# Kernel tuning notes

Hardware: AMD Instinct MI355X
Metric: run time of the kernel (lower is better)

## Reference

```python
import jax, jax.numpy as jnp
from jax import lax
import numpy as np

B, N_VARS, M_CLAUSES, K_DIM = 1024, 64, 256, 12
MAX_ITER = 12


def setup_inputs() -> dict:
    key = jax.random.key(0)
    k1, k2, k3, k4 = jax.random.split(key, 4)
    z = jax.random.uniform(k1, (B, N_VARS), dtype=jnp.float32)          # input probabilities
    S = jax.random.normal(k2, (M_CLAUSES, N_VARS + 1), dtype=jnp.float32) * 0.2  # learnable clause matrix (col 0 = truth var)
    w = jax.random.uniform(k3, (M_CLAUSES,), dtype=jnp.float32)          # learnable clause weights
    r = jax.random.normal(k4, (B, N_VARS, K_DIM), dtype=jnp.float32)     # random init directions
    return {"z": z, "S": S, "w": w, "r": r, "max_iter": MAX_ITER}


def _mixing(z, S, w, r, max_iter):
    Bsz, n = z.shape
    m, N = S.shape  # N = n + 1 (truth variable is column 0)
    k = r.shape[-1]
    eps = jnp.float32(1e-8)

    # truth direction v_T = e_0
    vT = jnp.zeros((k,), dtype=z.dtype).at[0].set(1.0)

    # random unit directions orthogonal to v_T (zero out component along e_0)
    r_perp = r.at[..., 0].set(0.0)
    r_perp = r_perp / jnp.maximum(jnp.linalg.norm(r_perp, axis=-1, keepdims=True), eps)

    # SATNet init: v_i = -cos(pi z_i) v_T + sin(pi z_i) r_perp_i
    ang = jnp.pi * z
    Vvars = -jnp.cos(ang)[..., None] * vT + jnp.sin(ang)[..., None] * r_perp  # [B,n,k]
    V = jnp.concatenate([jnp.broadcast_to(vT, (Bsz, 1, k)), Vvars], axis=1)   # [B,N,k]

    Sw = S * w[:, None]                       # weighted clause matrix [m,N]
    W = jnp.einsum('mn,bnk->bmk', Sw, V)      # running product Sw @ V, [B,m,k]
    snrm = jnp.sum(Sw * Sw, axis=0)           # ||s_i||^2 per variable, [N]

    def coord_step(carry, i):
        V, W = carry
        s_i = Sw[:, i]                         # [m]
        v_old = V[:, i, :]                     # [B,k]
        g = jnp.einsum('bmk,m->bk', W, s_i) - snrm[i] * v_old
        v_new = -g / jnp.maximum(jnp.linalg.norm(g, axis=-1, keepdims=True), eps)
        W = W + (v_new - v_old)[:, None, :] * s_i[None, :, None]  # rank-1 update
        V = V.at[:, i, :].set(v_new)
        return (V, W), None

    def sweep(carry, _):
        carry, _ = lax.scan(coord_step, carry, jnp.arange(1, N))  # coordinate descent over variables
        return carry, None

    (V, _), _ = lax.scan(sweep, (V, W), None, length=max_iter)

    # output probabilities: z_i = arccos(-v_i . v_T) / pi
    cos = jnp.clip(-V[:, 1:, 0], -1.0 + 1e-6, 1.0 - 1e-6)
    return jnp.arccos(cos) / jnp.pi


def reference(z, S, w, r, max_iter):
    return _mixing(z, S, w, r, max_iter)
```

## Files before the change

kernel.cpp:

```cpp
#include <hip/hip_runtime.h>
#include <math.h>

#define BATCH 1024
#define NV    64
#define MC    256
#define KD    12
#define PI_F  3.14159265358979323846f

#define CBUF  4480
#define C0OFF 4352
#define DGOFF 4416

template <int CTRL>
__device__ __forceinline__ float dpp_addf(float x) {
  int y = __builtin_amdgcn_update_dpp(0, __float_as_int(x), CTRL, 0xF, 0xF, true);
  return x + __int_as_float(y);
}
__device__ __forceinline__ float allreduce16(float x) {
  x = dpp_addf<0xB1>(x);
  x = dpp_addf<0x4E>(x);
  x = dpp_addf<0x124>(x);
  x = dpp_addf<0x128>(x);
  return x;
}
__device__ __forceinline__ float readlane63(float x) {
  return __int_as_float(__builtin_amdgcn_readlane(__float_as_int(x), 63));
}

__global__ void compute_C_kernel(const float* __restrict__ S,
                                 const float* __restrict__ w,
                                 float* __restrict__ Cg, int nsplit) {
  const int q = blockIdx.x;
  const int mc = blockIdx.y;
  const int j = threadIdx.x;
  if (j > NV) return;
  const int v = (q + 1) % 64 + 1;
  const int mlen = MC / nsplit;
  const int m0 = mc * mlen;
  float a0 = 0.f, a1 = 0.f, a2 = 0.f, a3 = 0.f;
  for (int m = m0; m < m0 + mlen; m += 4) {
    const float w0 = w[m], w1 = w[m + 1], w2 = w[m + 2], w3 = w[m + 3];
    a0 = fmaf(S[(m + 0) * (NV + 1) + v] * w0 * w0, S[(m + 0) * (NV + 1) + j], a0);
    a1 = fmaf(S[(m + 1) * (NV + 1) + v] * w1 * w1, S[(m + 1) * (NV + 1) + j], a1);
    a2 = fmaf(S[(m + 2) * (NV + 1) + v] * w2 * w2, S[(m + 2) * (NV + 1) + j], a2);
    a3 = fmaf(S[(m + 3) * (NV + 1) + v] * w3 * w3, S[(m + 3) * (NV + 1) + j], a3);
  }
  const float acc = (a0 + a1) + (a2 + a3);
  float* buf = Cg + mc * CBUF;
  if (j == 0) buf[C0OFF + q] = acc;
  else        buf[q * 68 + (j - 1)] = acc;
  const int pv = (v == 1) ? 64 : (v - 1);
  if (j == pv) buf[DGOFF + (v - 1)] = acc;
}

__global__ __launch_bounds__(256, 1) void mixing_kernel(
    const float* __restrict__ z, const float* __restrict__ r,
    const float* __restrict__ Cg, const int* __restrict__ max_iter_p,
    float* __restrict__ out, int nsplit) {
  __shared__ float Ls[CBUF];

  const int t = threadIdx.x;
  const int l = t & 63;
  const int kq = l >> 4;
  const int n16 = l & 15;
  const int b = blockIdx.x * 4 + (t >> 6);
  const int max_iter = max_iter_p[0];

  {
    const float4* src = (const float4*)Cg;
    float4* dst = (float4*)Ls;
    for (int idx = t; idx < CBUF / 4; idx += 256) {
      float4 a = src[idx];
      for (int u = 1; u < nsplit; ++u) {
        const float4 p = src[u * (CBUF / 4) + idx];
        a.x += p.x; a.y += p.y; a.z += p.z; a.w += p.w;
      }
      dst[idx] = a;
    }
  }

  const float row0 = (kq == 0) ? 1.f : 0.f;

  float V[4][3];
  #pragma unroll
  for (int s = 0; s < 4; ++s) {
    const int n = 4 * n16 + s;
    const float zv = z[b * NV + n];
    float rp[3];
    float ssp = 0.f;
    #pragma unroll
    for (int j = 0; j < 3; ++j) {
      const int k = 3 * kq + j;
      rp[j] = (k == 0) ? 0.f : r[(b * NV + n) * KD + k];
      ssp = fmaf(rp[j], rp[j], ssp);
    }
    ssp += __shfl_xor(ssp, 16, 64);
    ssp += __shfl_xor(ssp, 32, 64);
    const float inv = 1.f / fmaxf(sqrtf(ssp), 1e-8f);
    float sn, cs;
    sincosf(PI_F * zv, &sn, &cs);
    #pragma unroll
    for (int j = 0; j < 3; ++j) {
      const int k = 3 * kq + j;
      V[s][j] = (k == 0) ? -cs : sn * rp[j] * inv;
    }
  }

  __syncthreads();

  const float4* C4  = (const float4*)Ls;
  const float4* C04 = (const float4*)(Ls + C0OFF);
  const float4* Dg4 = (const float4*)(Ls + DGOFF);

  float P[3], vprev[3];

  auto prefetch = [&](float4 cb[4], float4& c0b, float4& dgb, int g) {
    #pragma unroll
    for (int s = 0; s < 4; ++s) cb[s] = C4[(4 * g + s) * 17 + n16];
    c0b = C04[g];
    dgb = Dg4[g];
  };

  auto do_group = [&](int ii, const float4 cb[4], const float4& c0b,
                      const float4& dgb) {
    const bool own  = (n16 == ii);
    const bool ownN = (n16 == ((ii + 1) & 15));
    const float* c0p = &c0b.x;
    const float* dgp = &dgb.x;
    #pragma unroll
    for (int s = 0; s < 4; ++s) {
      const float g0 = fmaf(dgp[s], vprev[0], P[0]);
      const float g1 = fmaf(dgp[s], vprev[1], P[1]);
      const float g2 = fmaf(dgp[s], vprev[2], P[2]);
      float n2p = g0 * g0;
      n2p = fmaf(g1, g1, n2p);
      n2p = fmaf(g2, g2, n2p);
      n2p = dpp_addf<0x142>(n2p);
      n2p = dpp_addf<0x143>(n2p);
      const float n2 = readlane63(n2p);
      const float inv = rsqrtf(fmaxf(n2, 1e-16f));
      const float v0 = -g0 * inv, v1 = -g1 * inv, v2 = -g2 * inv;
      V[s][0] = own ? v0 : V[s][0];
      V[s][1] = own ? v1 : V[s][1];
      V[s][2] = own ? v2 : V[s][2];

      float4 ce = cb[s];
      if (s == 0) { ce.x = own ? 0.f : ce.x; ce.y = own ? 0.f : ce.y; }
      if (s == 1) { ce.y = own ? 0.f : ce.y; ce.z = own ? 0.f : ce.z; }
      if (s == 2) { ce.z = own ? 0.f : ce.z; ce.w = own ? 0.f : ce.w; }
      if (s == 3) { ce.w = own ? 0.f : ce.w; ce.x = ownN ? 0.f : ce.x; }
      float p0 = ce.x * V[0][0];
      float p1 = ce.x * V[0][1];
      float p2 = ce.x * V[0][2];
      p0 = fmaf(ce.y, V[1][0], p0); p1 = fmaf(ce.y, V[1][1], p1); p2 = fmaf(ce.y, V[1][2], p2);
      p0 = fmaf(ce.z, V[2][0], p0); p1 = fmaf(ce.z, V[2][1], p1); p2 = fmaf(ce.z, V[2][2], p2);
      p0 = fmaf(ce.w, V[3][0], p0); p1 = fmaf(ce.w, V[3][1], p1); p2 = fmaf(ce.w, V[3][2], p2);
      p0 = allreduce16(p0);
      p1 = allreduce16(p1);
      p2 = allreduce16(p2);
      p0 = fmaf(row0, c0p[s], p0);
      P[0] = p0; P[1] = p1; P[2] = p2;
      vprev[0] = v0; vprev[1] = v1; vprev[2] = v2;
    }
  };

  float4 cbA[4], cbB[4], c0A, c0B, dgA, dgB;
  prefetch(cbA, c0A, dgA, 0);
  {
    float4 ce = C4[63 * 17 + n16];
    const float c0 = Ls[C0OFF + 63];
    ce.x = (n16 == 0) ? 0.f : ce.x;
    float p0 = ce.x * V[0][0];
    float p1 = ce.x * V[0][1];
    float p2 = ce.x * V[0][2];
    p0 = fmaf(ce.y, V[1][0], p0); p1 = fmaf(ce.y, V[1][1], p1); p2 = fmaf(ce.y, V[1][2], p2);
    p0 = fmaf(ce.z, V[2][0], p0); p1 = fmaf(ce.z, V[2][1], p1); p2 = fmaf(ce.z, V[2][2], p2);
    p0 = fmaf(ce.w, V[3][0], p0); p1 = fmaf(ce.w, V[3][1], p1); p2 = fmaf(ce.w, V[3][2], p2);
    p0 = allreduce16(p0);
    p1 = allreduce16(p1);
    p2 = allreduce16(p2);
    p0 = fmaf(row0, c0, p0);
    P[0] = p0; P[1] = p1; P[2] = p2;
    vprev[0] = 0.f; vprev[1] = 0.f; vprev[2] = 0.f;
  }

  for (int it = 0; it < max_iter; ++it) {
    for (int ih = 0; ih < 8; ++ih) {
      prefetch(cbB, c0B, dgB, 2 * ih + 1);
      do_group(2 * ih, cbA, c0A, dgA);
      prefetch(cbA, c0A, dgA, (2 * ih + 2) & 15);
      do_group(2 * ih + 1, cbB, c0B, dgB);
    }
  }

  if (kq == 0) {
    float4 o;
    float* op = &o.x;
    #pragma unroll
    for (int s = 0; s < 4; ++s) {
      float cv = -V[s][0];
      cv = fminf(fmaxf(cv, -1.f + 1e-6f), 1.f - 1e-6f);
      op[s] = acosf(cv) * (1.f / PI_F);
    }
    ((float4*)(out + b * NV))[n16] = o;
  }
}

extern "C" void kernel_launch(void* const* d_in, const int* in_sizes, int n_in,
                              void* d_out, int out_size, void* d_ws, size_t ws_size,
                              hipStream_t stream) {
  const float* z = (const float*)d_in[0];
  const float* S = (const float*)d_in[1];
  const float* w = (const float*)d_in[2];
  const float* r = (const float*)d_in[3];
  const int* max_iter = (const int*)d_in[4];
  float* Cg = (float*)d_ws;

  const int nsplit = (ws_size >= (size_t)4 * CBUF * 4) ? 4 : 1;
  compute_C_kernel<<<dim3(NV, nsplit), 128, 0, stream>>>(S, w, Cg, nsplit);
  mixing_kernel<<<BATCH / 4, 256, 0, stream>>>(z, r, Cg, max_iter,
                                               (float*)d_out, nsplit);
}
```

Baseline: 164.2 us.

## Delay each coordinate's V write by one step to break the serial dependency chain

The coordinate-descent step is reordered so that the partial product for the next variable is computed from V values that are one update stale. The missing contribution is patched in with a second diagonal coefficient term (DgB), giving a two-deep correction with vp1 and vp2. This takes the norm, rsqrt and V update off the critical path before the cross-lane allreduce, so the reductions for consecutive coordinates can overlap. It also switches to the raw rsq builtin. The cost is an extra precomputed coefficient table and more masking logic, with some numerical and correctness risk in the bookkeeping.

```diff
diff --git a/kernel.cpp b/kernel.cpp
--- a/kernel.cpp
+++ b/kernel.cpp
@@ -7,9 +7,10 @@
 #define KD    12
 #define PI_F  3.14159265358979323846f
 
-#define CBUF  4480
-#define C0OFF 4352
-#define DGOFF 4416
+#define CBUF   4544
+#define C0OFF  4352
+#define DGAOFF 4416
+#define DGBOFF 4480
 
 template <int CTRL>
 __device__ __forceinline__ float dpp_addf(float x) {
@@ -49,8 +50,10 @@
   float* buf = Cg + mc * CBUF;
   if (j == 0) buf[C0OFF + q] = acc;
   else        buf[q * 68 + (j - 1)] = acc;
-  const int pv = (v == 1) ? 64 : (v - 1);
-  if (j == pv) buf[DGOFF + (v - 1)] = acc;
+  const int p1 = (v == 1) ? 64 : (v - 1);
+  const int p2 = (v == 1) ? 63 : (v == 2) ? 64 : (v - 2);
+  if (j == p1) buf[DGAOFF + (v - 1)] = acc;
+  if (j == p2) buf[DGBOFF + (v - 1)] = acc;
 }
 
 __global__ __launch_bounds__(256, 1) void mixing_kernel(
@@ -108,89 +111,121 @@
 
   __syncthreads();
 
-  const float4* C4  = (const float4*)Ls;
-  const float4* C04 = (const float4*)(Ls + C0OFF);
-  const float4* Dg4 = (const float4*)(Ls + DGOFF);
-
-  float P[3], vprev[3];
-
-  auto prefetch = [&](float4 cb[4], float4& c0b, float4& dgb, int g) {
+  const float4* C4   = (const float4*)Ls;
+  const float4* C04  = (const float4*)(Ls + C0OFF);
+  const float4* DgA4 = (const float4*)(Ls + DGAOFF);
+  const float4* DgB4 = (const float4*)(Ls + DGBOFF);
+
+  float P[3], vp1[3], vp2[3];
+
+  {
+    float4 ce = C4[63 * 17 + n16];
+    const float c0 = Ls[C0OFF + 63];
+    const bool l15 = (n16 == 15), l0 = (n16 == 0);
+    ce.z = l15 ? 0.f : ce.z;
+    ce.w = l15 ? 0.f : ce.w;
+    ce.x = l0 ? 0.f : ce.x;
+    float q0 = ce.x * V[0][0];
+    float q1 = ce.x * V[0][1];
+    float q2 = ce.x * V[0][2];
+    q0 = fmaf(ce.y, V[1][0], q0); q1 = fmaf(ce.y, V[1][1], q1); q2 = fmaf(ce.y, V[1][2], q2);
+    q0 = fmaf(ce.z, V[2][0], q0); q1 = fmaf(ce.z, V[2][1], q1); q2 = fmaf(ce.z, V[2][2], q2);
+    q0 = fmaf(ce.w, V[3][0], q0); q1 = fmaf(ce.w, V[3][1], q1); q2 = fmaf(ce.w, V[3][2], q2);
+    q0 = allreduce16(q0);
+    q1 = allreduce16(q1);
+    q2 = allreduce16(q2);
+    q0 = fmaf(row0, c0, q0);
+    P[0] = q0; P[1] = q1; P[2] = q2;
+    const int src = l | 15;
+    #pragma unroll
+    for (int j = 0; j < 3; ++j) {
+      vp1[j] = __shfl(V[3][j], src, 64);
+      vp2[j] = __shfl(V[2][j], src, 64);
+    }
+  }
+
+  float4 cbA[4], cbB[4], c0A, c0B, daA, daB, dbA, dbB;
+
+  auto prefetch = [&](float4 cb[4], float4& c0b, float4& dab, float4& dbb, int g) {
     #pragma unroll
     for (int s = 0; s < 4; ++s) cb[s] = C4[(4 * g + s) * 17 + n16];
     c0b = C04[g];
-    dgb = Dg4[g];
+    dab = DgA4[g];
+    dbb = DgB4[g];
   };
 
   auto do_group = [&](int ii, const float4 cb[4], const float4& c0b,
-                      const float4& dgb) {
+                      const float4& dab, const float4& dbb) {
     const bool own  = (n16 == ii);
+    const bool ownP = (n16 == ((ii + 15) & 15));
     const bool ownN = (n16 == ((ii + 1) & 15));
     const float* c0p = &c0b.x;
-    const float* dgp = &dgb.x;
+    const float* dap = &dab.x;
+    const float* dbp = &dbb.x;
     #pragma unroll
     for (int s = 0; s < 4; ++s) {
-      const float g0 = fmaf(dgp[s], vprev[0], P[0]);
-      const float g1 = fmaf(dgp[s], vprev[1], P[1]);
-      const float g2 = fmaf(dgp[s], vprev[2], P[2]);
-      float n2p = g0 * g0;
-      n2p = fmaf(g1, g1, n2p);
-      n2p = fmaf(g2, g2, n2p);
+      float4 ce = cb[s];
+      if (s == 0) { ce.w = ownP ? 0.f : ce.w; ce.x = own ? 0.f : ce.x; ce.y = own ? 0.f : ce.y; }
+      if (s == 1) { ce.x = own ? 0.f : ce.x;  ce.y = own ? 0.f : ce.y; ce.z = own ? 0.f : ce.z; }
+      if (s == 2) { ce.y = own ? 0.f : ce.y;  ce.z = own ? 0.f : ce.z; ce.w = own ? 0.f : ce.w; }
+      if (s == 3) { ce.z = own ? 0.f : ce.z;  ce.w = own ? 0.f : ce.w; ce.x = ownN ? 0.f : ce.x; }
+      float q0 = ce.x * V[0][0];
+      float q1 = ce.x * V[0][1];
+      float q2 = ce.x * V[0][2];
+      q0 = fmaf(ce.y, V[1][0], q0); q1 = fmaf(ce.y, V[1][1], q1); q2 = fmaf(ce.y, V[1][2], q2);
+      q0 = fmaf(ce.z, V[2][0], q0); q1 = fmaf(ce.z, V[2][1], q1); q2 = fmaf(ce.z, V[2][2], q2);
+      q0 = fmaf(ce.w, V[3][0], q0); q1 = fmaf(ce.w, V[3][1], q1); q2 = fmaf(ce.w, V[3][2], q2);
+      q0 = allreduce16(q0);
+      q1 = allreduce16(q1);
+      q2 = allreduce16(q2);
+      q0 = fmaf(row0, c0p[s], q0);
+
+      float g0 = fmaf(dbp[s], vp2[0], P[0]);
+      float g1 = fmaf(dbp[s], vp2[1], P[1]);
+      float g2 = fmaf(dbp[s], vp2[2], P[2]);
+      g0 = fmaf(dap[s], vp1[0], g0);
+      g1 = fmaf(dap[s], vp1[1], g1);
+      g2 = fmaf(dap[s], vp1[2], g2);
+      const float t0 = g0 * g0, t1 = g1 * g1, t2 = g2 * g2;
+      float n2p = (t0 + t1) + t2;
       n2p = dpp_addf<0x142>(n2p);
       n2p = dpp_addf<0x143>(n2p);
       const float n2 = readlane63(n2p);
-      const float inv = rsqrtf(fmaxf(n2, 1e-16f));
+      const float inv = __builtin_amdgcn_rsqf(fmaxf(n2, 1e-16f));
       const float v0 = -g0 * inv, v1 = -g1 * inv, v2 = -g2 * inv;
-      V[s][0] = own ? v0 : V[s][0];
-      V[s][1] = own ? v1 : V[s][1];
-      V[s][2] = own ? v2 : V[s][2];
-
-      float4 ce = cb[s];
-      if (s == 0) { ce.x = own ? 0.f : ce.x; ce.y = own ? 0.f : ce.y; }
-      if (s == 1) { ce.y = own ? 0.f : ce.y; ce.z = own ? 0.f : ce.z; }
-      if (s == 2) { ce.z = own ? 0.f : ce.z; ce.w = own ? 0.f : ce.w; }
-      if (s == 3) { ce.w = own ? 0.f : ce.w; ce.x = ownN ? 0.f : ce.x; }
-      float p0 = ce.x * V[0][0];
-      float p1 = ce.x * V[0][1];
-      float p2 = ce.x * V[0][2];
-      p0 = fmaf(ce.y, V[1][0], p0); p1 = fmaf(ce.y, V[1][1], p1); p2 = fmaf(ce.y, V[1][2], p2);
-      p0 = fmaf(ce.z, V[2][0], p0); p1 = fmaf(ce.z, V[2][1], p1); p2 = fmaf(ce.z, V[2][2], p2);
-      p0 = fmaf(ce.w, V[3][0], p0); p1 = fmaf(ce.w, V[3][1], p1); p2 = fmaf(ce.w, V[3][2], p2);
-      p0 = allreduce16(p0);
-      p1 = allreduce16(p1);
-      p2 = allreduce16(p2);
-      p0 = fmaf(row0, c0p[s], p0);
-      P[0] = p0; P[1] = p1; P[2] = p2;
-      vprev[0] = v0; vprev[1] = v1; vprev[2] = v2;
+
+      if (s == 0) {
+        V[3][0] = ownP ? vp1[0] : V[3][0];
+        V[3][1] = ownP ? vp1[1] : V[3][1];
+        V[3][2] = ownP ? vp1[2] : V[3][2];
+      } else {
+        V[s - 1][0] = own ? vp1[0] : V[s - 1][0];
+        V[s - 1][1] = own ? vp1[1] : V[s - 1][1];
+        V[s - 1][2] = own ? vp1[2] : V[s - 1][2];
+      }
+
+      vp2[0] = vp1[0]; vp2[1] = vp1[1]; vp2[2] = vp1[2];
+      vp1[0] = v0;     vp1[1] = v1;     vp1[2] = v2;
+      P[0] = q0; P[1] = q1; P[2] = q2;
     }
   };
 
-  float4 cbA[4], cbB[4], c0A, c0B, dgA, dgB;
-  prefetch(cbA, c0A, dgA, 0);
-  {
-    float4 ce = C4[63 * 17 + n16];
-    const float c0 = Ls[C0OFF + 63];
-    ce.x = (n16 == 0) ? 0.f : ce.x;
-    float p0 = ce.x * V[0][0];
-    float p1 = ce.x * V[0][1];
-    float p2 = ce.x * V[0][2];
-    p0 = fmaf(ce.y, V[1][0], p0); p1 = fmaf(ce.y, V[1][1], p1); p2 = fmaf(ce.y, V[1][2], p2);
-    p0 = fmaf(ce.z, V[2][0], p0); p1 = fmaf(ce.z, V[2][1], p1); p2 = fmaf(ce.z, V[2][2], p2);
-    p0 = fmaf(ce.w, V[3][0], p0); p1 = fmaf(ce.w, V[3][1], p1); p2 = fmaf(ce.w, V[3][2], p2);
-    p0 = allreduce16(p0);
-    p1 = allreduce16(p1);
-    p2 = allreduce16(p2);
-    p0 = fmaf(row0, c0, p0);
-    P[0] = p0; P[1] = p1; P[2] = p2;
-    vprev[0] = 0.f; vprev[1] = 0.f; vprev[2] = 0.f;
-  }
+  prefetch(cbA, c0A, daA, dbA, 0);
 
   for (int it = 0; it < max_iter; ++it) {
     for (int ih = 0; ih < 8; ++ih) {
-      prefetch(cbB, c0B, dgB, 2 * ih + 1);
-      do_group(2 * ih, cbA, c0A, dgA);
-      prefetch(cbA, c0A, dgA, (2 * ih + 2) & 15);
-      do_group(2 * ih + 1, cbB, c0B, dgB);
-    }
+      prefetch(cbB, c0B, daB, dbB, 2 * ih + 1);
+      do_group(2 * ih, cbA, c0A, daA, dbA);
+      prefetch(cbA, c0A, daA, dbA, (2 * ih + 2) & 15);
+      do_group(2 * ih + 1, cbB, c0B, daB, dbB);
+    }
+  }
+
+  {
+    const bool l15 = (n16 == 15);
+    V[3][0] = l15 ? vp1[0] : V[3][0];
+    V[3][1] = l15 ? vp1[1] : V[3][1];
+    V[3][2] = l15 ? vp1[2] : V[3][2];
   }
 
   if (kq == 0) {
```

Result: faster. 158.9 us (-3.2%).

## Maintain per-variable gradient vectors with rank-1 updates instead of recomputing dot products

Applied to the files above, without the earlier changes.

Replaces the per-coordinate recomputation of the gradient (a 64-term dot product followed by three 16-lane allreduces) with a persistent per-lane gradient array G that gets a rank-1 update after each variable changes. The next variable's gradient and old vector are fetched ahead of time with ds_bpermute, which takes the cross-lane reductions off the serial dependency chain. The C-matrix layout is rebuilt with separate diagonal tables, and compute_C uses more split partitions when workspace allows. In exchange it adds an initial full G computation, more registers, and possible accumulated drift in G over iterations.

```diff
diff --git a/kernel.cpp b/kernel.cpp
--- a/kernel.cpp
+++ b/kernel.cpp
@@ -7,9 +7,10 @@
 #define KD    12
 #define PI_F  3.14159265358979323846f
 
-#define CBUF  4480
+#define CBUF  4544
 #define C0OFF 4352
-#define DGOFF 4416
+#define DIOFF 4416
+#define DGOFF 4480
 
 template <int CTRL>
 __device__ __forceinline__ float dpp_addf(float x) {
@@ -25,6 +26,9 @@
 }
 __device__ __forceinline__ float readlane63(float x) {
   return __int_as_float(__builtin_amdgcn_readlane(__float_as_int(x), 63));
+}
+__device__ __forceinline__ float bperm(int byteidx, float x) {
+  return __int_as_float(__builtin_amdgcn_ds_bpermute(byteidx, __float_as_int(x)));
 }
 
 __global__ void compute_C_kernel(const float* __restrict__ S,
@@ -34,7 +38,7 @@
   const int mc = blockIdx.y;
   const int j = threadIdx.x;
   if (j > NV) return;
-  const int v = (q + 1) % 64 + 1;
+  const int v = q + 1;
   const int mlen = MC / nsplit;
   const int m0 = mc * mlen;
   float a0 = 0.f, a1 = 0.f, a2 = 0.f, a3 = 0.f;
@@ -47,10 +51,11 @@
   }
   const float acc = (a0 + a1) + (a2 + a3);
   float* buf = Cg + mc * CBUF;
+  const int p1 = (v == 1) ? 64 : (v - 1);
   if (j == 0) buf[C0OFF + q] = acc;
-  else        buf[q * 68 + (j - 1)] = acc;
-  const int pv = (v == 1) ? 64 : (v - 1);
-  if (j == pv) buf[DGOFF + (v - 1)] = acc;
+  if (j == v) buf[DIOFF + q] = acc;
+  if (j == p1) buf[DGOFF + q] = acc;
+  if (j > 0) buf[q * 68 + (j - 1)] = acc;
 }
 
 __global__ __launch_bounds__(256, 1) void mixing_kernel(
@@ -109,87 +114,117 @@
   __syncthreads();
 
   const float4* C4  = (const float4*)Ls;
-  const float4* C04 = (const float4*)(Ls + C0OFF);
+  const float4* Di4 = (const float4*)(Ls + DIOFF);
   const float4* Dg4 = (const float4*)(Ls + DGOFF);
 
-  float P[3], vprev[3];
-
-  auto prefetch = [&](float4 cb[4], float4& c0b, float4& dgb, int g) {
+  float G[4][3] = {{0.f,0.f,0.f},{0.f,0.f,0.f},{0.f,0.f,0.f},{0.f,0.f,0.f}};
+  for (int q16 = 0; q16 < 16; ++q16) {
+    const bool ow = (n16 == q16);
+    #pragma unroll
+    for (int s = 0; s < 4; ++s) {
+      const int q = 4 * q16 + s;
+      const float4 ce = C4[q * 17 + n16];
+      float q0 = ce.x * V[0][0];
+      float q1 = ce.x * V[0][1];
+      float q2 = ce.x * V[0][2];
+      q0 = fmaf(ce.y, V[1][0], q0); q1 = fmaf(ce.y, V[1][1], q1); q2 = fmaf(ce.y, V[1][2], q2);
+      q0 = fmaf(ce.z, V[2][0], q0); q1 = fmaf(ce.z, V[2][1], q1); q2 = fmaf(ce.z, V[2][2], q2);
+      q0 = fmaf(ce.w, V[3][0], q0); q1 = fmaf(ce.w, V[3][1], q1); q2 = fmaf(ce.w, V[3][2], q2);
+      q0 = allreduce16(q0);
+      q1 = allreduce16(q1);
+      q2 = allreduce16(q2);
+      q0 = fmaf(row0, Ls[C0OFF + q], q0);
+      G[s][0] = ow ? q0 : G[s][0];
+      G[s][1] = ow ? q1 : G[s][1];
+      G[s][2] = ow ? q2 : G[s][2];
+    }
+  }
+
+  const int bpbase = (l & 48) << 2;
+
+  float4 cbA[4], cbB[4], diA, diB, dgA, dgB;
+  auto prefetch = [&](float4 cb[4], float4& dib, float4& dgb, int g) {
     #pragma unroll
     for (int s = 0; s < 4; ++s) cb[s] = C4[(4 * g + s) * 17 + n16];
-    c0b = C04[g];
+    dib = Di4[g];
     dgb = Dg4[g];
   };
 
-  auto do_group = [&](int ii, const float4 cb[4], const float4& c0b,
-                      const float4& dgb) {
-    const bool own  = (n16 == ii);
-    const bool ownN = (n16 == ((ii + 1) & 15));
-    const float* c0p = &c0b.x;
+  float bp[3], vo[3], d[3];
+
+  prefetch(cbA, diA, dgA, 0);
+
+  {
+    float gp0 = fmaf(-diA.x, V[0][0], G[0][0]);
+    float gp1 = fmaf(-diA.x, V[0][1], G[0][1]);
+    float gp2 = fmaf(-diA.x, V[0][2], G[0][2]);
+    bp[0] = bperm(bpbase, gp0);
+    bp[1] = bperm(bpbase, gp1);
+    bp[2] = bperm(bpbase, gp2);
+    vo[0] = bperm(bpbase, V[0][0]);
+    vo[1] = bperm(bpbase, V[0][1]);
+    vo[2] = bperm(bpbase, V[0][2]);
+    d[0] = 0.f; d[1] = 0.f; d[2] = 0.f;
+  }
+
+  auto do_group = [&](int ii, const float4 cb[4], const float4& dib,
+                      const float4& dgb, float diNextX) {
+    const bool own = (n16 == ii);
+    const float* dip = &dib.x;
     const float* dgp = &dgb.x;
+    const int idxC = bpbase + 4 * ii;
+    const int idxN = bpbase + ((4 * ii + 4) & 63);
     #pragma unroll
     for (int s = 0; s < 4; ++s) {
-      const float g0 = fmaf(dgp[s], vprev[0], P[0]);
-      const float g1 = fmaf(dgp[s], vprev[1], P[1]);
-      const float g2 = fmaf(dgp[s], vprev[2], P[2]);
-      float n2p = g0 * g0;
-      n2p = fmaf(g1, g1, n2p);
-      n2p = fmaf(g2, g2, n2p);
+      const int snext = (s + 1) & 3;
+      const float diag_n = (s < 3) ? dip[s + 1] : diNextX;
+      const int idx = (s < 3) ? idxC : idxN;
+
+      const float gp0 = fmaf(-diag_n, V[snext][0], G[snext][0]);
+      const float gp1 = fmaf(-diag_n, V[snext][1], G[snext][1]);
+      const float gp2 = fmaf(-diag_n, V[snext][2], G[snext][2]);
+      const float bpn0 = bperm(idx, gp0);
+      const float bpn1 = bperm(idx, gp1);
+      const float bpn2 = bperm(idx, gp2);
+      const float von0 = bperm(idx, V[snext][0]);
+      const float von1 = bperm(idx, V[snext][1]);
+      const float von2 = bperm(idx, V[snext][2]);
+
+      const float gg0 = fmaf(dgp[s], d[0], bp[0]);
+      const float gg1 = fmaf(dgp[s], d[1], bp[1]);
+      const float gg2 = fmaf(dgp[s], d[2], bp[2]);
+      float n2p = gg0 * gg0;
+      n2p = fmaf(gg1, gg1, n2p);
+      n2p = fmaf(gg2, gg2, n2p);
       n2p = dpp_addf<0x142>(n2p);
       n2p = dpp_addf<0x143>(n2p);
       const float n2 = readlane63(n2p);
-      const float inv = rsqrtf(fmaxf(n2, 1e-16f));
-      const float v0 = -g0 * inv, v1 = -g1 * inv, v2 = -g2 * inv;
-      V[s][0] = own ? v0 : V[s][0];
-      V[s][1] = own ? v1 : V[s][1];
-      V[s][2] = own ? v2 : V[s][2];
-
-      float4 ce = cb[s];
-      if (s == 0) { ce.x = own ? 0.f : ce.x; ce.y = own ? 0.f : ce.y; }
-      if (s == 1) { ce.y = own ? 0.f : ce.y; ce.z = own ? 0.f : ce.z; }
-      if (s == 2) { ce.z = own ? 0.f : ce.z; ce.w = own ? 0.f : ce.w; }
-      if (s == 3) { ce.w = own ? 0.f : ce.w; ce.x = ownN ? 0.f : ce.x; }
-      float p0 = ce.x * V[0][0];
-      float p1 = ce.x * V[0][1];
-      float p2 = ce.x * V[0][2];
-      p0 = fmaf(ce.y, V[1][0], p0); p1 = fmaf(ce.y, V[1][1], p1); p2 = fmaf(ce.y, V[1][2], p2);
-      p0 = fmaf(ce.z, V[2][0], p0); p1 = fmaf(ce.z, V[2][1], p1); p2 = fmaf(ce.z, V[2][2], p2);
-      p0 = fmaf(ce.w, V[3][0], p0); p1 = fmaf(ce.w, V[3][1], p1); p2 = fmaf(ce.w, V[3][2], p2);
-      p0 = allreduce16(p0);
-      p1 = allreduce16(p1);
-      p2 = allreduce16(p2);
-      p0 = fmaf(row0, c0p[s], p0);
-      P[0] = p0; P[1] = p1; P[2] = p2;
-      vprev[0] = v0; vprev[1] = v1; vprev[2] = v2;
+      const float inv = __builtin_amdgcn_rsqf(fmaxf(n2, 1e-16f));
+      const float vn0 = -gg0 * inv, vn1 = -gg1 * inv, vn2 = -gg2 * inv;
+      const float dn0 = vn0 - vo[0], dn1 = vn1 - vo[1], dn2 = vn2 - vo[2];
+
+      V[s][0] = own ? vn0 : V[s][0];
+      V[s][1] = own ? vn1 : V[s][1];
+      V[s][2] = own ? vn2 : V[s][2];
+
+      const float4 ce = cb[s];
+      G[0][0] = fmaf(ce.x, dn0, G[0][0]); G[0][1] = fmaf(ce.x, dn1, G[0][1]); G[0][2] = fmaf(ce.x, dn2, G[0][2]);
+      G[1][0] = fmaf(ce.y, dn0, G[1][0]); G[1][1] = fmaf(ce.y, dn1, G[1][1]); G[1][2] = fmaf(ce.y, dn2, G[1][2]);
+      G[2][0] = fmaf(ce.z, dn0, G[2][0]); G[2][1] = fmaf(ce.z, dn1, G[2][1]); G[2][2] = fmaf(ce.z, dn2, G[2][2]);
+      G[3][0] = fmaf(ce.w, dn0, G[3][0]); G[3][1] = fmaf(ce.w, dn1, G[3][1]); G[3][2] = fmaf(ce.w, dn2, G[3][2]);
+
+      bp[0] = bpn0; bp[1] = bpn1; bp[2] = bpn2;
+      vo[0] = von0; vo[1] = von1; vo[2] = von2;
+      d[0] = dn0;   d[1] = dn1;   d[2] = dn2;
     }
   };
-
-  float4 cbA[4], cbB[4], c0A, c0B, dgA, dgB;
-  prefetch(cbA, c0A, dgA, 0);
-  {
-    float4 ce = C4[63 * 17 + n16];
-    const float c0 = Ls[C0OFF + 63];
-    ce.x = (n16 == 0) ? 0.f : ce.x;
-    float p0 = ce.x * V[0][0];
-    float p1 = ce.x * V[0][1];
-    float p2 = ce.x * V[0][2];
-    p0 = fmaf(ce.y, V[1][0], p0); p1 = fmaf(ce.y, V[1][1], p1); p2 = fmaf(ce.y, V[1][2], p2);
-    p0 = fmaf(ce.z, V[2][0], p0); p1 = fmaf(ce.z, V[2][1], p1); p2 = fmaf(ce.z, V[2][2], p2);
-    p0 = fmaf(ce.w, V[3][0], p0); p1 = fmaf(ce.w, V[3][1], p1); p2 = fmaf(ce.w, V[3][2], p2);
-    p0 = allreduce16(p0);
-    p1 = allreduce16(p1);
-    p2 = allreduce16(p2);
-    p0 = fmaf(row0, c0, p0);
-    P[0] = p0; P[1] = p1; P[2] = p2;
-    vprev[0] = 0.f; vprev[1] = 0.f; vprev[2] = 0.f;
-  }
 
   for (int it = 0; it < max_iter; ++it) {
     for (int ih = 0; ih < 8; ++ih) {
-      prefetch(cbB, c0B, dgB, 2 * ih + 1);
-      do_group(2 * ih, cbA, c0A, dgA);
-      prefetch(cbA, c0A, dgA, (2 * ih + 2) & 15);
-      do_group(2 * ih + 1, cbB, c0B, dgB);
+      prefetch(cbB, diB, dgB, 2 * ih + 1);
+      do_group(2 * ih, cbA, diA, dgA, diB.x);
+      prefetch(cbA, diA, dgA, (2 * ih + 2) & 15);
+      do_group(2 * ih + 1, cbB, diB, dgB, diA.x);
     }
   }
 
@@ -216,7 +251,8 @@
   const int* max_iter = (const int*)d_in[4];
   float* Cg = (float*)d_ws;
 
-  const int nsplit = (ws_size >= (size_t)4 * CBUF * 4) ? 4 : 1;
+  const int nsplit = (ws_size >= (size_t)8 * CBUF * 4) ? 8
+                   : (ws_size >= (size_t)4 * CBUF * 4) ? 4 : 1;
   compute_C_kernel<<<dim3(NV, nsplit), 128, 0, stream>>>(S, w, Cg, nsplit);
   mixing_kernel<<<BATCH / 4, 256, 0, stream>>>(z, r, Cg, max_iter,
                                                (float*)d_out, nsplit);
```

Measured after the change: 168.4 us. +2.5%, slower.
